# Optimization experiments

Measured on AMD Instinct MI355X. Metric: run time of the kernel, lower is better.

## Reference

```python
import jax, jax.numpy as jnp
import numpy as np

B, S, E, H = 1, 2048, 1024, 16
D = E // H  # head_dim = 64
MAX_POS = 2048
NEG_INF = -1e30


def _rotary(x):
    # x: [B, S, H, D]; positions along axis 1
    half = D // 2
    inv_freq = 1.0 / (10000.0 ** (jnp.arange(0, D, 2, dtype=jnp.float32) / D))  # [D/2]
    freqs = jnp.arange(S, dtype=jnp.float32)[:, None] * inv_freq[None, :]       # [S, D/2]
    emb = jnp.concatenate([freqs, freqs], axis=-1)                              # [S, D]
    cos = jnp.cos(emb)[None, :, None, :]
    sin = jnp.sin(emb)[None, :, None, :]
    x1, x2 = x[..., :half], x[..., half:]
    rot = jnp.concatenate([-x2, x1], axis=-1)
    return x * cos + rot * sin


def setup_inputs() -> dict:
    key = jax.random.key(0)
    ks = jax.random.split(key, 8)
    w = lambda k: (jax.random.normal(k, (E, E), jnp.float32) * 0.02)
    inp = {
        "x": jax.random.normal(ks[0], (B, S, E), jnp.float32),
        "mask": jnp.tril(jnp.ones((S, S), jnp.int32)),  # causal 0/1 mask
        "Wq": w(ks[1]), "bq": jnp.zeros((E,), jnp.float32),
        "Wk": w(ks[2]), "bk": jnp.zeros((E,), jnp.float32),
        "Wv": w(ks[3]), "bv": jnp.zeros((E,), jnp.float32),
        "Wo": w(ks[4]), "bo": jnp.zeros((E,), jnp.float32),
        "rel_pos_emb": jax.random.normal(ks[5], (2 * MAX_POS - 1, D), jnp.float32) * 0.02,
    }
    return inp


def reference(x, mask, Wq, bq, Wk, bk, Wv, bv, Wo, bo, rel_pos_emb):
    scale = D ** -0.5
    q = (x @ Wq + bq).reshape(B, S, H, D)
    k = (x @ Wk + bk).reshape(B, S, H, D)
    v = (x @ Wv + bv).reshape(B, S, H, D)
    q = _rotary(q)
    k = _rotary(k)
    # [B, H, S, D]
    qh = jnp.swapaxes(q, 1, 2)
    kh = jnp.swapaxes(k, 1, 2)
    vh = jnp.swapaxes(v, 1, 2)
    scores = jnp.einsum('bhid,bhjd->bhij', qh, kh) * scale  # [B,H,S,S]
    # relative position bias (Shaw-style: gather then contract with q)
    pos = jnp.arange(S)
    bucket = pos[None, :] - pos[:, None] + S - 1            # [S,S] in [0, 2S-2]
    rel = rel_pos_emb[bucket]                               # [S,S,D]
    scores = scores + jnp.einsum('bhid,ijd->bhij', qh, rel)
    scores = jnp.where(mask[None, None, :, :] == 0, NEG_INF, scores)
    attn = jax.nn.softmax(scores, axis=-1)
    out = jnp.einsum('bhij,bhjd->bhid', attn, vh)           # [B,H,S,D]
    out = jnp.swapaxes(out, 1, 2).reshape(B, S, E)
    return out @ Wo + bo
```

## Files before the change

kernel.cpp:

```cpp
#include <hip/hip_runtime.h>
#include <hip/hip_bf16.h>

typedef __attribute__((ext_vector_type(8))) short bf16x8;
typedef __attribute__((ext_vector_type(4))) float f32x4;

#define MFMA16(a,b,c) __builtin_amdgcn_mfma_f32_16x16x32_bf16((a),(b),(c),0,0,0)
#define GLDS16(g, l) __builtin_amdgcn_global_load_lds((const __attribute__((address_space(1))) void*)(g), (__attribute__((address_space(3))) void*)(l), 16, 0, 0)

static constexpr int S_ = 2048, E_ = 1024, H_ = 16;
static constexpr float QS = 0.125f * 1.44269504f;

__device__ __forceinline__ unsigned pk2(float a, float b) {
  __hip_bfloat16 ba = __float2bfloat16(a), bb = __float2bfloat16(b);
  return (unsigned)*(unsigned short*)&ba | ((unsigned)*(unsigned short*)&bb << 16);
}
__device__ __forceinline__ float ubf(unsigned short u) {
  return __uint_as_float((unsigned)u << 16);
}

__global__ __launch_bounds__(256) void prep_k(const float* __restrict__ x, const float* __restrict__ rel,
                                              const float* __restrict__ Wq, const float* __restrict__ Wk,
                                              const float* __restrict__ Wv, const float* __restrict__ Wo,
                                              const float* __restrict__ bq, const float* __restrict__ bk,
                                              const float* __restrict__ bv,
                                              __hip_bfloat16* __restrict__ xb, __hip_bfloat16* __restrict__ relb,
                                              __hip_bfloat16* __restrict__ wqkvT, __hip_bfloat16* __restrict__ woT,
                                              float* __restrict__ bqkv, float* __restrict__ cost,
                                              float* __restrict__ sint) {
  int blk = blockIdx.x, tid = threadIdx.x;
  if (blk < 1024) {
    __shared__ float tile[64][65];
    int wsel = blk >> 8, sub = blk & 255;
    const float* W = wsel == 0 ? Wq : wsel == 1 ? Wk : wsel == 2 ? Wv : Wo;
    __hip_bfloat16* WT = wsel < 3 ? wqkvT + (size_t)wsel * E_ * E_ : woT;
    int bx = sub & 15, by = sub >> 4;
    for (int i = tid; i < 4096; i += 256) {
      int ki = i >> 6, ni = i & 63;
      tile[ki][ni] = W[(size_t)(by*64 + ki) * E_ + bx*64 + ni];
    }
    __syncthreads();
    for (int i = tid; i < 4096; i += 256) {
      int ni = i >> 6, ki = i & 63;
      WT[(size_t)(bx*64 + ni) * E_ + by*64 + ki] = __float2bfloat16(tile[ki][ni]);
    }
  } else if (blk < 3072) {
    int i = (blk - 1024) * 256 + tid;
    float4 v = reinterpret_cast<const float4*>(x)[i];
    xb[4*i+0] = __float2bfloat16(v.x);
    xb[4*i+1] = __float2bfloat16(v.y);
    xb[4*i+2] = __float2bfloat16(v.z);
    xb[4*i+3] = __float2bfloat16(v.w);
  } else if (blk < 3328) {
    int i = (blk - 3072) * 256 + tid;
    if (i < 65520) {
      float4 v = reinterpret_cast<const float4*>(rel)[i];
      relb[4*i+0] = __float2bfloat16(v.x * 8.f);
      relb[4*i+1] = __float2bfloat16(v.y * 8.f);
      relb[4*i+2] = __float2bfloat16(v.z * 8.f);
      relb[4*i+3] = __float2bfloat16(v.w * 8.f);
    }
  } else if (blk < 3584) {
    int idx = (blk - 3328) * 256 + tid;
    int f = idx & 31, s = idx >> 5;
    float inv = powf(10000.f, -(float)f * (1.f/32.f));
    float a = (float)s * inv;
    cost[idx] = cosf(a);
    sint[idx] = sinf(a);
  } else {
    int i = (blk - 3584) * 256 + tid;
    if (i < 3072) bqkv[i] = i < 1024 ? bq[i] : (i < 2048 ? bk[i-1024] : bv[i-2048]);
  }
}

template<int BM, int MODE>
__global__ __launch_bounds__(256) void gemm_k(const __hip_bfloat16* __restrict__ A,
                                              const __hip_bfloat16* __restrict__ BT,
                                              const float* __restrict__ bias,
                                              const float* __restrict__ cost,
                                              const float* __restrict__ sint,
                                              __hip_bfloat16* __restrict__ qhh,
                                              __hip_bfloat16* __restrict__ khh,
                                              __hip_bfloat16* __restrict__ vt,
                                              float* __restrict__ outf,
                                              int K) {
  constexpr int MI = BM/32;
  __shared__ __hip_bfloat16 As[2][BM*64];
  __shared__ __hip_bfloat16 Bs[2][128*64];
  int tid = threadIdx.x, lane = tid & 63, w = tid >> 6;
  int rowq = lane & 15, hi = lane >> 4, ksel = hi << 3;
  int wr = (w >> 1) * (BM/2), wc = (w & 1) * 64;
  int m0 = blockIdx.y * BM, n0 = blockIdx.x * 128;
  int l3 = lane >> 3, l7 = lane & 7;
  f32x4 acc[MI][4] = {};

  auto stage = [&](int k0, int buf) {
    const char* Ap = (const char*)A + ((size_t)(m0 + w*(BM/4)) * K + k0) * 2;
    const char* Bp = (const char*)BT + ((size_t)(n0 + w*32) * K + k0) * 2;
    char* Ad = (char*)&As[buf][w*(BM/4)*64];
    char* Bd = (char*)&Bs[buf][w*32*64];
    for (int i = 0; i < MI; ++i)
      GLDS16(Ap + (size_t)(i*8 + l3)*(K*2) + l7*16, Ad + i*1024);
    for (int i = 0; i < 4; ++i)
      GLDS16(Bp + (size_t)(i*8 + l3)*(K*2) + l7*16, Bd + i*1024);
  };

  stage(0, 0);
  __syncthreads();
  int buf = 0;
  int nk = K >> 6;
  for (int t = 0; t < nk; ++t) {
    if (t + 1 < nk) stage((t+1)*64, buf^1);
    for (int kk = 0; kk < 64; kk += 32) {
      bf16x8 a[MI], b[4];
      for (int i = 0; i < MI; ++i) a[i] = *(const bf16x8*)&As[buf][(wr + i*16 + rowq)*64 + kk + ksel];
      for (int j = 0; j < 4; ++j)  b[j] = *(const bf16x8*)&Bs[buf][(wc + j*16 + rowq)*64 + kk + ksel];
      for (int i = 0; i < MI; ++i)
        for (int j = 0; j < 4; ++j)
          acc[i][j] = MFMA16(a[i], b[j], acc[i][j]);
    }
    __syncthreads();
    buf ^= 1;
  }

  if constexpr (MODE == 0) {
    int matsel = n0 >> 10, ncol = n0 & 1023;
    float bcol[4];
    for (int j = 0; j < 4; ++j) bcol[j] = bias[n0 + wc + j*16 + rowq];
    if (matsel < 2) {
      __hip_bfloat16* dst = matsel ? khh : qhh;
      float qs = matsel ? 1.0f : QS;
      for (int i = 0; i < MI; ++i)
        for (int rg = 0; rg < 4; ++rg) {
          int s = m0 + wr + i*16 + hi*4 + rg;
          for (int j = 0; j < 2; ++j) {
            int colp = ncol + wc + j*16 + rowq;
            int hh = colp >> 6, f = colp & 31;
            float c = cost[s*32 + f], sn = sint[s*32 + f];
            float v1 = acc[i][j][rg]   + bcol[j];
            float v2 = acc[i][j+2][rg] + bcol[j+2];
            dst[((size_t)hh*S_ + s)*64 + f]      = __float2bfloat16((v1*c - v2*sn) * qs);
            dst[((size_t)hh*S_ + s)*64 + f + 32] = __float2bfloat16((v2*c + v1*sn) * qs);
          }
        }
    } else {
      for (int i = 0; i < MI; ++i)
        for (int j = 0; j < 4; ++j) {
          int colp = ncol + wc + j*16 + rowq;
          int hh = colp >> 6, d = colp & 63;
          int s0b = m0 + wr + i*16 + hi*4;
          __hip_bfloat16 tmp[4];
          for (int rg = 0; rg < 4; ++rg)
            tmp[rg] = __float2bfloat16(acc[i][j][rg] + bcol[j]);
          *(ushort4*)(vt + ((size_t)hh*64 + d)*S_ + s0b) = *(ushort4*)tmp;
        }
    }
  } else {
    for (int i = 0; i < MI; ++i)
      for (int rg = 0; rg < 4; ++rg) {
        int row = m0 + wr + i*16 + hi*4 + rg;
        for (int j = 0; j < 4; ++j) {
          int col = n0 + wc + j*16 + rowq;
          outf[(size_t)row*E_ + col] = acc[i][j][rg] + bias[col];
        }
      }
  }
}

__global__ __launch_bounds__(256,2) void attn_k(const __hip_bfloat16* __restrict__ qh,
                                                const __hip_bfloat16* __restrict__ kh,
                                                const __hip_bfloat16* __restrict__ vt,
                                                const __hip_bfloat16* __restrict__ relb,
                                                __hip_bfloat16* __restrict__ opart,
                                                float2* __restrict__ ml) {
  int h = blockIdx.x & 15, p = (blockIdx.x >> 4) & 15, r = blockIdx.x >> 8;
  int tid = threadIdx.x, lane = tid & 63, w = tid >> 6;
  int rowq = lane & 15, hi = lane >> 4, ksel = hi << 3;
  int l3 = lane >> 3, l7 = lane & 7;
  int swz = (l7*16) ^ (l3 << 4);
  __shared__ __hip_bfloat16 Ks[2][4096];
  __shared__ __hip_bfloat16 Vs[2][4096];
  __shared__ char WPb[4][4096];
  char* wp = WPb[w] + rowq*256;
  int sw8 = (rowq & 7) << 4;
  int pcol0 = ((hi*16)      ^ ((rowq & 7) << 4)) >> 1;
  int pcol1 = ((64 + hi*16) ^ ((rowq & 7) << 4)) >> 1;

  int T0 = p + 1;
  int g0 = r*11, g1 = g0 + 11;

  for (int seg = 0; seg < 2; ++seg) {
    int qb, t0, t1;
    if (seg == 0) { qb = p;      t0 = g0;                          t1 = g1 < T0 ? g1 : T0; }
    else          { qb = 31 - p; t0 = (g0 > T0 ? g0 : T0) - T0;    t1 = g1 - T0; }
    int i0w = qb*64 + w*16;

    const __hip_bfloat16* qrow = qh + ((size_t)h*S_ + i0w + rowq)*64 + ksel;
    bf16x8 q0 = *(const bf16x8*)(qrow);
    bf16x8 q1 = *(const bf16x8*)(qrow + 32);
    f32x4 o[4] = {};
    float m = -1e30f, l = 0.f;

    auto stage = [&](int t, int buf) {
      int j0 = t * 64;
      const char* kp = (const char*)(kh + ((size_t)h*S_ + j0 + w*16)*64);
      const char* vp = (const char*)(vt + ((size_t)(h*64 + w*16))*S_ + j0);
      char* kd = (char*)&Ks[buf][w*16*64];
      char* vd = (char*)&Vs[buf][w*16*64];
      for (int i = 0; i < 2; ++i) {
        GLDS16(kp + (size_t)(i*8 + l3)*128  + swz, kd + i*1024);
        GLDS16(vp + (size_t)(i*8 + l3)*4096 + swz, vd + i*1024);
      }
    };
    auto ldrel = [&](int t, bf16x8* rr) {
      const __hip_bfloat16* rp = relb + (size_t)(t*64 - i0w + 2032 + rowq)*64 + ksel;
      #pragma unroll
      for (int nf = 0; nf < 5; ++nf) {
        rr[nf*2]   = *(const bf16x8*)(rp + nf*1024);
        rr[nf*2+1] = *(const bf16x8*)(rp + nf*1024 + 32);
      }
    };

    if (t0 < t1) {
      bf16x8 rc[10], rn[10];
      ldrel(t0, rc);
      stage(t0, 0);
      __syncthreads();
      int buf = 0;
      for (int t = t0; t < t1; ++t) {
        bool more = (t + 1 < t1);
        if (more) { stage(t+1, buf^1); ldrel(t+1, rn); }

        f32x4 sa[4] = {};
        f32x4 wt[5] = {};
        __builtin_amdgcn_s_setprio(1);
        for (int kk = 0; kk < 2; ++kk) {
          bf16x8 qf = kk ? q1 : q0;
          int pc = kk ? pcol1 : pcol0;
          for (int nf = 0; nf < 4; ++nf) {
            bf16x8 kf = *(const bf16x8*)&Ks[buf][(nf*16 + rowq)*64 + pc];
            sa[nf] = MFMA16(kf, qf, sa[nf]);
          }
          for (int nf = 0; nf < 5; ++nf)
            wt[nf] = MFMA16(rc[nf*2+kk], qf, wt[nf]);
        }
        __builtin_amdgcn_s_setprio(0);

        #pragma unroll
        for (int nf = 0; nf < 5; ++nf) {
          uint2 u = { pk2(wt[nf][0], wt[nf][1]), pk2(wt[nf][2], wt[nf][3]) };
          *(uint2*)(wp + ((nf*32 + hi*8) ^ sw8)) = u;
        }

        float sv[4][4];
        float tm = -1e30f;
        bool diag = (t == qb);
        #pragma unroll
        for (int nf = 0; nf < 4; ++nf)
          #pragma unroll
          for (int rg = 0; rg < 4; ++rg) {
            int kl = nf*16 + hi*4 + rg;
            float v = sa[nf][rg] + ubf(*(const unsigned short*)(wp + ((2*kl + 30 - 2*rowq) ^ sw8)));
            if (diag && kl > w*16 + rowq) v = -1e30f;
            sv[nf][rg] = v;
            tm = fmaxf(tm, v);
          }
        tm = fmaxf(tm, __shfl_xor(tm, 16));
        tm = fmaxf(tm, __shfl_xor(tm, 32));
        float mnew = fmaxf(m, tm);
        float al = exp2f(m - mnew);
        m = mnew;
        float ls = 0.f;
        float pe[4][4];
        #pragma unroll
        for (int nf = 0; nf < 4; ++nf)
          #pragma unroll
          for (int rg = 0; rg < 4; ++rg) {
            float e = exp2f(sv[nf][rg] - mnew);
            pe[nf][rg] = e;
            ls += e;
          }
        l = l * al + ls;
        #pragma unroll
        for (int nf = 0; nf < 4; ++nf) {
          uint2 u = { pk2(pe[nf][0], pe[nf][1]), pk2(pe[nf][2], pe[nf][3]) };
          *(uint2*)(wp + ((nf*32 + hi*8) ^ sw8)) = u;
        }
        float alq[4];
        #pragma unroll
        for (int rg = 0; rg < 4; ++rg) alq[rg] = __shfl(al, hi*4 + rg, 16);
        #pragma unroll
        for (int df = 0; df < 4; ++df)
          #pragma unroll
          for (int rg = 0; rg < 4; ++rg) o[df][rg] *= alq[rg];

        __builtin_amdgcn_s_setprio(1);
        for (int kk = 0; kk < 2; ++kk) {
          bf16x8 a = *(const bf16x8*)(wp + ((kk*64 + hi*16) ^ sw8));
          int pc = kk ? pcol1 : pcol0;
          for (int df = 0; df < 4; ++df) {
            bf16x8 b = *(const bf16x8*)&Vs[buf][(df*16 + rowq)*64 + pc];
            o[df] = MFMA16(a, b, o[df]);
          }
        }
        __builtin_amdgcn_s_setprio(0);
        __syncthreads();
        buf ^= 1;
        if (more) {
          #pragma unroll
          for (int i = 0; i < 10; ++i) rc[i] = rn[i];
        }
      }
    }

    float lt = l;
    lt += __shfl_xor(lt, 16);
    lt += __shfl_xor(lt, 32);
    if (lane < 16) ml[((size_t)r*S_ + i0w + rowq)*H_ + h] = make_float2(m, lt);
    #pragma unroll
    for (int df = 0; df < 4; ++df)
      #pragma unroll
      for (int rg = 0; rg < 4; ++rg)
        opart[(size_t)r*S_*E_ + (size_t)(i0w + hi*4 + rg)*E_ + h*64 + df*16 + rowq] =
            __float2bfloat16(o[df][rg]);
    __syncthreads();
  }
}

__global__ __launch_bounds__(256) void combine_k(const __hip_bfloat16* __restrict__ opart,
                                                 const float2* __restrict__ ml,
                                                 __hip_bfloat16* __restrict__ aout) {
  int r = blockIdx.x, tid = threadIdx.x;
  int c = tid * 4, h = c >> 6;
  float2 a0 = ml[(size_t)r*H_ + h];
  float2 a1 = ml[((size_t)S_ + r)*H_ + h];
  float2 a2 = ml[((size_t)2*S_ + r)*H_ + h];
  float M = fmaxf(fmaxf(a0.x, a1.x), a2.x);
  float w0 = exp2f(a0.x - M), w1 = exp2f(a1.x - M), w2 = exp2f(a2.x - M);
  float dinv = 1.0f / (w0*a0.y + w1*a1.y + w2*a2.y);
  w0 *= dinv; w1 *= dinv; w2 *= dinv;
  const unsigned short* ob = (const unsigned short*)opart + (size_t)r*E_ + c;
  ushort4 u0 = *(const ushort4*)ob;
  ushort4 u1 = *(const ushort4*)(ob + (size_t)S_*E_);
  ushort4 u2 = *(const ushort4*)(ob + (size_t)2*S_*E_);
  __hip_bfloat16 res[4];
  res[0] = __float2bfloat16(w0*ubf(u0.x) + w1*ubf(u1.x) + w2*ubf(u2.x));
  res[1] = __float2bfloat16(w0*ubf(u0.y) + w1*ubf(u1.y) + w2*ubf(u2.y));
  res[2] = __float2bfloat16(w0*ubf(u0.z) + w1*ubf(u1.z) + w2*ubf(u2.z));
  res[3] = __float2bfloat16(w0*ubf(u0.w) + w1*ubf(u1.w) + w2*ubf(u2.w));
  *(ushort4*)((unsigned short*)aout + (size_t)r*E_ + c) = *(ushort4*)res;
}

extern "C" void kernel_launch(void* const* d_in, const int* in_sizes, int n_in,
                              void* d_out, int out_size, void* d_ws, size_t ws_size,
                              hipStream_t stream) {
  const float* x   = (const float*)d_in[0];
  const float* Wq  = (const float*)d_in[2];
  const float* bq  = (const float*)d_in[3];
  const float* Wk  = (const float*)d_in[4];
  const float* bk  = (const float*)d_in[5];
  const float* Wv  = (const float*)d_in[6];
  const float* bv  = (const float*)d_in[7];
  const float* Wo  = (const float*)d_in[8];
  const float* bo  = (const float*)d_in[9];
  const float* rel = (const float*)d_in[10];
  float* out = (float*)d_out;

  char* ws = (char*)d_ws;
  size_t off = 0;
  auto alloc = [&](size_t bytes) -> void* {
    void* p = ws + off;
    off = (off + bytes + 255) & ~(size_t)255;
    return p;
  };
  __hip_bfloat16* xb    = (__hip_bfloat16*)alloc((size_t)S_*E_*2);
  __hip_bfloat16* wqkvT = (__hip_bfloat16*)alloc((size_t)3*E_*E_*2);
  float* cost = (float*)alloc((size_t)S_*32*4);
  float* sint = (float*)alloc((size_t)S_*32*4);
  float* bqkv = (float*)alloc((size_t)3072*4);
  if (off < (size_t)16*1024*1024) off = (size_t)16*1024*1024;
  __hip_bfloat16* woT   = (__hip_bfloat16*)alloc((size_t)E_*E_*2);
  __hip_bfloat16* relb  = (__hip_bfloat16*)alloc((size_t)4095*64*2);
  __hip_bfloat16* qhh  = (__hip_bfloat16*)alloc((size_t)S_*E_*2);
  __hip_bfloat16* khh  = (__hip_bfloat16*)alloc((size_t)S_*E_*2);
  __hip_bfloat16* vth  = (__hip_bfloat16*)alloc((size_t)S_*E_*2);
  __hip_bfloat16* aout = (__hip_bfloat16*)alloc((size_t)S_*E_*2);
  float2* ml = (float2*)alloc((size_t)3*S_*H_*8);

  __hip_bfloat16* opart = (__hip_bfloat16*)ws;

  prep_k<<<3596, 256, 0, stream>>>(x, rel, Wq, Wk, Wv, Wo, bq, bk, bv,
                                   xb, relb, wqkvT, woT, bqkv, cost, sint);

  gemm_k<64,0><<<dim3(24,32), 256, 0, stream>>>(xb, wqkvT, bqkv, cost, sint,
                                                qhh, khh, vth, nullptr, E_);

  attn_k<<<768, 256, 0, stream>>>(qhh, khh, vth, relb, opart, ml);
  combine_k<<<S_, 256, 0, stream>>>(opart, ml, aout);

  gemm_k<64,1><<<dim3(8,32), 256, 0, stream>>>(aout, woT, bo, nullptr, nullptr,
                                               nullptr, nullptr, nullptr, out, E_);
}
```

Before: 132.7 us.

## Use 128-row query tiles with 8 waves sharing K/V staging, split keys four ways

The attention kernel moves from 256-thread blocks covering 64 query rows to 512-thread blocks covering 128 query rows. All eight waves share each staged 64-key K/V tile, which halves the global-to-LDS traffic per query row. The key range is now split into four partitions instead of three, with a matching four-way combine and a larger ml buffer. The relative-position register double buffer is dropped and the next tile's rel loads are issued mid-iteration to cut register pressure, which allows launch bounds of 512 threads and 4 blocks. The risks are more LDS per block, lower latency hiding for the rel loads, and imbalance from the different causal-tile partitioning.

```diff
diff --git a/kernel.cpp b/kernel.cpp
--- a/kernel.cpp
+++ b/kernel.cpp
@@ -166,33 +166,34 @@
   }
 }
 
-__global__ __launch_bounds__(256,2) void attn_k(const __hip_bfloat16* __restrict__ qh,
+__global__ __launch_bounds__(512,4) void attn_k(const __hip_bfloat16* __restrict__ qh,
                                                 const __hip_bfloat16* __restrict__ kh,
                                                 const __hip_bfloat16* __restrict__ vt,
                                                 const __hip_bfloat16* __restrict__ relb,
                                                 __hip_bfloat16* __restrict__ opart,
                                                 float2* __restrict__ ml) {
-  int h = blockIdx.x & 15, p = (blockIdx.x >> 4) & 15, r = blockIdx.x >> 8;
+  int h = blockIdx.x & 15, p = (blockIdx.x >> 4) & 7, r = blockIdx.x >> 7;
   int tid = threadIdx.x, lane = tid & 63, w = tid >> 6;
   int rowq = lane & 15, hi = lane >> 4, ksel = hi << 3;
   int l3 = lane >> 3, l7 = lane & 7;
   int swz = (l7*16) ^ (l3 << 4);
   __shared__ __hip_bfloat16 Ks[2][4096];
   __shared__ __hip_bfloat16 Vs[2][4096];
-  __shared__ char WPb[4][4096];
+  __shared__ char WPb[8][4096];
   char* wp = WPb[w] + rowq*256;
   int sw8 = (rowq & 7) << 4;
   int pcol0 = ((hi*16)      ^ ((rowq & 7) << 4)) >> 1;
   int pcol1 = ((64 + hi*16) ^ ((rowq & 7) << 4)) >> 1;
 
-  int T0 = p + 1;
-  int g0 = r*11, g1 = g0 + 11;
+  int T0 = 2*p + 2;
+  int g0 = (34*r) >> 2, g1 = (34*(r+1)) >> 2;
 
   for (int seg = 0; seg < 2; ++seg) {
     int qb, t0, t1;
-    if (seg == 0) { qb = p;      t0 = g0;                          t1 = g1 < T0 ? g1 : T0; }
-    else          { qb = 31 - p; t0 = (g0 > T0 ? g0 : T0) - T0;    t1 = g1 - T0; }
-    int i0w = qb*64 + w*16;
+    if (seg == 0) { qb = p;      t0 = g0;                        t1 = g1 < T0 ? g1 : T0; }
+    else          { qb = 15 - p; t0 = (g0 > T0 ? g0 : T0) - T0;  t1 = g1 - T0; }
+    int i0w = qb*128 + w*16;
+    int td = 2*qb + (w >> 2);
 
     const __hip_bfloat16* qrow = qh + ((size_t)h*S_ + i0w + rowq)*64 + ksel;
     bf16x8 q0 = *(const bf16x8*)(qrow);
@@ -202,14 +203,10 @@
 
     auto stage = [&](int t, int buf) {
       int j0 = t * 64;
-      const char* kp = (const char*)(kh + ((size_t)h*S_ + j0 + w*16)*64);
-      const char* vp = (const char*)(vt + ((size_t)(h*64 + w*16))*S_ + j0);
-      char* kd = (char*)&Ks[buf][w*16*64];
-      char* vd = (char*)&Vs[buf][w*16*64];
-      for (int i = 0; i < 2; ++i) {
-        GLDS16(kp + (size_t)(i*8 + l3)*128  + swz, kd + i*1024);
-        GLDS16(vp + (size_t)(i*8 + l3)*4096 + swz, vd + i*1024);
-      }
+      const char* kp = (const char*)(kh + ((size_t)h*S_ + j0 + w*8)*64);
+      const char* vp = (const char*)(vt + ((size_t)(h*64 + w*8))*S_ + j0);
+      GLDS16(kp + (size_t)l3*128  + swz, (char*)&Ks[buf][w*8*64]);
+      GLDS16(vp + (size_t)l3*4096 + swz, (char*)&Vs[buf][w*8*64]);
     };
     auto ldrel = [&](int t, bf16x8* rr) {
       const __hip_bfloat16* rp = relb + (size_t)(t*64 - i0w + 2032 + rowq)*64 + ksel;
@@ -221,14 +218,14 @@
     };
 
     if (t0 < t1) {
-      bf16x8 rc[10], rn[10];
+      bf16x8 rc[10];
       ldrel(t0, rc);
       stage(t0, 0);
       __syncthreads();
       int buf = 0;
       for (int t = t0; t < t1; ++t) {
         bool more = (t + 1 < t1);
-        if (more) { stage(t+1, buf^1); ldrel(t+1, rn); }
+        if (more) stage(t+1, buf^1);
 
         f32x4 sa[4] = {};
         f32x4 wt[5] = {};
@@ -251,19 +248,33 @@
           *(uint2*)(wp + ((nf*32 + hi*8) ^ sw8)) = u;
         }
 
+        if (more) ldrel(t+1, rc);
+
         float sv[4][4];
         float tm = -1e30f;
-        bool diag = (t == qb);
-        #pragma unroll
-        for (int nf = 0; nf < 4; ++nf)
+        if (t >= td) {
+          int lim = i0w + rowq - t*64;
           #pragma unroll
-          for (int rg = 0; rg < 4; ++rg) {
-            int kl = nf*16 + hi*4 + rg;
-            float v = sa[nf][rg] + ubf(*(const unsigned short*)(wp + ((2*kl + 30 - 2*rowq) ^ sw8)));
-            if (diag && kl > w*16 + rowq) v = -1e30f;
-            sv[nf][rg] = v;
-            tm = fmaxf(tm, v);
-          }
+          for (int nf = 0; nf < 4; ++nf)
+            #pragma unroll
+            for (int rg = 0; rg < 4; ++rg) {
+              int kl = nf*16 + hi*4 + rg;
+              float v = sa[nf][rg] + ubf(*(const unsigned short*)(wp + ((2*kl + 30 - 2*rowq) ^ sw8)));
+              if (kl > lim) v = -1e30f;
+              sv[nf][rg] = v;
+              tm = fmaxf(tm, v);
+            }
+        } else {
+          #pragma unroll
+          for (int nf = 0; nf < 4; ++nf)
+            #pragma unroll
+            for (int rg = 0; rg < 4; ++rg) {
+              int kl = nf*16 + hi*4 + rg;
+              float v = sa[nf][rg] + ubf(*(const unsigned short*)(wp + ((2*kl + 30 - 2*rowq) ^ sw8)));
+              sv[nf][rg] = v;
+              tm = fmaxf(tm, v);
+            }
+        }
         tm = fmaxf(tm, __shfl_xor(tm, 16));
         tm = fmaxf(tm, __shfl_xor(tm, 32));
         float mnew = fmaxf(m, tm);
@@ -305,10 +316,6 @@
         __builtin_amdgcn_s_setprio(0);
         __syncthreads();
         buf ^= 1;
-        if (more) {
-          #pragma unroll
-          for (int i = 0; i < 10; ++i) rc[i] = rn[i];
-        }
       }
     }
 
@@ -334,19 +341,22 @@
   float2 a0 = ml[(size_t)r*H_ + h];
   float2 a1 = ml[((size_t)S_ + r)*H_ + h];
   float2 a2 = ml[((size_t)2*S_ + r)*H_ + h];
-  float M = fmaxf(fmaxf(a0.x, a1.x), a2.x);
-  float w0 = exp2f(a0.x - M), w1 = exp2f(a1.x - M), w2 = exp2f(a2.x - M);
-  float dinv = 1.0f / (w0*a0.y + w1*a1.y + w2*a2.y);
-  w0 *= dinv; w1 *= dinv; w2 *= dinv;
+  float2 a3 = ml[((size_t)3*S_ + r)*H_ + h];
+  float M = fmaxf(fmaxf(a0.x, a1.x), fmaxf(a2.x, a3.x));
+  float w0 = exp2f(a0.x - M), w1 = exp2f(a1.x - M);
+  float w2 = exp2f(a2.x - M), w3 = exp2f(a3.x - M);
+  float dinv = 1.0f / (w0*a0.y + w1*a1.y + w2*a2.y + w3*a3.y);
+  w0 *= dinv; w1 *= dinv; w2 *= dinv; w3 *= dinv;
   const unsigned short* ob = (const unsigned short*)opart + (size_t)r*E_ + c;
   ushort4 u0 = *(const ushort4*)ob;
   ushort4 u1 = *(const ushort4*)(ob + (size_t)S_*E_);
   ushort4 u2 = *(const ushort4*)(ob + (size_t)2*S_*E_);
+  ushort4 u3 = *(const ushort4*)(ob + (size_t)3*S_*E_);
   __hip_bfloat16 res[4];
-  res[0] = __float2bfloat16(w0*ubf(u0.x) + w1*ubf(u1.x) + w2*ubf(u2.x));
-  res[1] = __float2bfloat16(w0*ubf(u0.y) + w1*ubf(u1.y) + w2*ubf(u2.y));
-  res[2] = __float2bfloat16(w0*ubf(u0.z) + w1*ubf(u1.z) + w2*ubf(u2.z));
-  res[3] = __float2bfloat16(w0*ubf(u0.w) + w1*ubf(u1.w) + w2*ubf(u2.w));
+  res[0] = __float2bfloat16(w0*ubf(u0.x) + w1*ubf(u1.x) + w2*ubf(u2.x) + w3*ubf(u3.x));
+  res[1] = __float2bfloat16(w0*ubf(u0.y) + w1*ubf(u1.y) + w2*ubf(u2.y) + w3*ubf(u3.y));
+  res[2] = __float2bfloat16(w0*ubf(u0.z) + w1*ubf(u1.z) + w2*ubf(u2.z) + w3*ubf(u3.z));
+  res[3] = __float2bfloat16(w0*ubf(u0.w) + w1*ubf(u1.w) + w2*ubf(u2.w) + w3*ubf(u3.w));
   *(ushort4*)((unsigned short*)aout + (size_t)r*E_ + c) = *(ushort4*)res;
 }
 
@@ -384,7 +394,7 @@
   __hip_bfloat16* khh  = (__hip_bfloat16*)alloc((size_t)S_*E_*2);
   __hip_bfloat16* vth  = (__hip_bfloat16*)alloc((size_t)S_*E_*2);
   __hip_bfloat16* aout = (__hip_bfloat16*)alloc((size_t)S_*E_*2);
-  float2* ml = (float2*)alloc((size_t)3*S_*H_*8);
+  float2* ml = (float2*)alloc((size_t)4*S_*H_*8);
 
   __hip_bfloat16* opart = (__hip_bfloat16*)ws;
 
@@ -394,7 +404,7 @@
   gemm_k<64,0><<<dim3(24,32), 256, 0, stream>>>(xb, wqkvT, bqkv, cost, sint,
                                                 qhh, khh, vth, nullptr, E_);
 
-  attn_k<<<768, 256, 0, stream>>>(qhh, khh, vth, relb, opart, ml);
+  attn_k<<<512, 512, 0, stream>>>(qhh, khh, vth, relb, opart, ml);
   combine_k<<<S_, 256, 0, stream>>>(opart, ml, aout);
 
   gemm_k<64,1><<<dim3(8,32), 256, 0, stream>>>(aout, woT, bo, nullptr, nullptr,
```

Measured after the change: 168.0 us. 1.27x slower.
